# Kernel tuning notes

Hardware: AMD Instinct MI355X
Metric: run time of the kernel (lower is better)

Reference implementation:

```python
import jax, jax.numpy as jnp
import numpy as np

N_NODES = 500_000
N_EDGES = 8_000_000
N_GRAPHS = 25_000
NUM_TASKS = 138
READOUT_DIM = 175
MLP_DIMS = (96, 63)
BN_EPS = 1e-5


def _linear_params(key, fan_in, fan_out):
    k1, k2 = jax.random.split(key)
    bound = 1.0 / np.sqrt(fan_in)
    W = jax.random.uniform(k1, (fan_in, fan_out), jnp.float32, -bound, bound)
    b = jax.random.uniform(k2, (fan_out,), jnp.float32, -bound, bound)
    return W, b


def setup_inputs() -> dict:
    key = jax.random.key(0)
    ks = jax.random.split(key, 16)
    inp = {}
    inp["x"] = jax.random.normal(ks[0], (N_NODES, 48), jnp.float32)
    inp["mol_features"] = jax.random.normal(ks[1], (N_GRAPHS, 10), jnp.float32)
    inp["edge_index"] = jax.random.randint(ks[2], (2, N_EDGES), 0, N_NODES, jnp.int32)
    inp["batch"] = jnp.sort(jax.random.randint(ks[3], (N_NODES,), 0, N_GRAPHS, jnp.int32))
    # GCN layer linears (message transform)
    inp["w_g1"], inp["b_g1"] = _linear_params(ks[4], 48, 20)
    inp["w_g2"], inp["b_g2"] = _linear_params(ks[5], 20, 27)
    inp["w_g3"], inp["b_g3"] = _linear_params(ks[6], 27, 36)
    inp["w_g4"], inp["b_g4"] = _linear_params(ks[7], 36, 36)
    # Readout linears
    inp["w_r1"], inp["b_r1"] = _linear_params(ks[8], 20, READOUT_DIM)
    inp["w_r2"], inp["b_r2"] = _linear_params(ks[9], 27, READOUT_DIM)
    inp["w_r3"], inp["b_r3"] = _linear_params(ks[10], 36, READOUT_DIM)
    inp["w_r4"], inp["b_r4"] = _linear_params(ks[11], 36, READOUT_DIM)
    # MLP
    inp["w_fc1"], inp["b_fc1"] = _linear_params(ks[12], READOUT_DIM + 10, MLP_DIMS[0])
    inp["bn1_g"] = jnp.ones((MLP_DIMS[0],), jnp.float32)
    inp["bn1_b"] = jnp.zeros((MLP_DIMS[0],), jnp.float32)
    inp["w_fc2"], inp["b_fc2"] = _linear_params(ks[13], MLP_DIMS[0], MLP_DIMS[1])
    inp["bn2_g"] = jnp.ones((MLP_DIMS[1],), jnp.float32)
    inp["bn2_b"] = jnp.zeros((MLP_DIMS[1],), jnp.float32)
    inp["w_out"], inp["b_out"] = _linear_params(ks[14], MLP_DIMS[1], NUM_TASKS)
    return inp


def _gcn(x, src, dst, W, b):
    # message: Linear on gathered source features; aggregate: scatter-max; update: SELU
    m = x[src] @ W + b                                  # [E, out]
    agg = jax.ops.segment_max(m, dst, num_segments=N_NODES)
    agg = jnp.where(jnp.isfinite(agg), agg, 0.0)        # PyG fills empty segments with 0
    return jax.nn.selu(agg)


def _readout(x, batch, W, b):
    return jax.ops.segment_sum(x, batch, num_segments=N_GRAPHS) @ W + b


def _bn(h, g, b):
    mu = h.mean(axis=0)
    var = h.var(axis=0)
    return g * (h - mu) / jnp.sqrt(var + BN_EPS) + b


def reference(x, mol_features, w_g1, b_g1, w_g2, b_g2, w_g3, b_g3, w_g4, b_g4,
              w_r1, b_r1, w_r2, b_r2, w_r3, b_r3, w_r4, b_r4,
              w_fc1, b_fc1, bn1_g, bn1_b, w_fc2, b_fc2, bn2_g, bn2_b,
              w_out, b_out, edge_index, batch):
    src, dst = edge_index[0], edge_index[1]
    x1 = _gcn(x, src, dst, w_g1, b_g1)
    x2 = _gcn(x1, src, dst, w_g2, b_g2)
    x3 = _gcn(x2, src, dst, w_g3, b_g3)
    x4 = _gcn(x3, src, dst, w_g4, b_g4)
    r = (_readout(x1, batch, w_r1, b_r1) + _readout(x2, batch, w_r2, b_r2)
         + _readout(x3, batch, w_r3, b_r3) + _readout(x4, batch, w_r4, b_r4))
    h = jnp.concatenate([r, mol_features], axis=1)      # [G, 185]
    h = jax.nn.relu(_bn(h @ w_fc1 + b_fc1, bn1_g, bn1_b))
    h = jax.nn.relu(_bn(h @ w_fc2 + b_fc2, bn2_g, bn2_b))
    return jax.nn.sigmoid(h @ w_out + b_out)            # [G, num_tasks]
```

## Files before the change

### kernel.cpp

```cpp
#include <hip/hip_runtime.h>
#include <hip/hip_fp16.h>
#include <math.h>

#define N_NODES  500000
#define N_EDGES  8000000
#define N_GRAPHS 25000
#define SD  119
#define RD  175
#define H1  96
#define H2  63
#define NT  138
#define GPB 16

#define B2SHIFT 11
#define B2NODES 2048
#define NBUCK2  245
#define BIN_CHUNK 4096
#define NB_BIN 1954
#define NBF 7813
#define CSR_CAP 1536

static __device__ __forceinline__ float selu_f(float m){
    const float scale=1.0507009873554805f, alpha=1.6732632423543772f;
    return m > 0.0f ? scale*m : scale*alpha*(__expf(m)-1.0f);
}

static __device__ __forceinline__ unsigned pkmax(unsigned a, unsigned b){
    unsigned r;
    asm volatile("v_pk_max_f16 %0, %1, %2" : "=v"(r) : "v"(a), "v"(b));
    return r;
}

static __device__ __forceinline__ float2 h2_to_f2(unsigned u){
    union{ unsigned u; __half2 h; } c; c.u = u;
    return __half22float2(c.h);
}

__global__ void k_init(int* chist, float* S){
    int i = blockIdx.x*256 + threadIdx.x;
    if(i < NBUCK2) chist[i] = 0;
    if(i < N_GRAPHS*SD) S[i] = 0.f;
}

__device__ __forceinline__ int block_excl_scan_256(int v){
    __shared__ int sh[256];
    int t = threadIdx.x;
    sh[t] = v; __syncthreads();
    int acc = v;
    for(int off=1; off<256; off<<=1){
        int add = (t>=off) ? sh[t-off] : 0;
        __syncthreads();
        acc += add;
        sh[t] = acc;
        __syncthreads();
    }
    return acc - v;
}

__global__ __launch_bounds__(256) void k_chist(const int* __restrict__ dst, int* __restrict__ chist){
    __shared__ int lh[256];
    int t = threadIdx.x;
    lh[t]=0; __syncthreads();
    int base = blockIdx.x*BIN_CHUNK;
    #pragma unroll
    for(int k=0;k<16;k++){
        int e = base + k*256 + t;
        if(e < N_EDGES) atomicAdd(&lh[dst[e]>>B2SHIFT], 1);
    }
    __syncthreads();
    if(t < NBUCK2 && lh[t]) atomicAdd(&chist[t], lh[t]);
}

__global__ void k_cscan(const int* __restrict__ chist, int* __restrict__ cptr, int* __restrict__ bcur){
    int t = threadIdx.x;
    int v = (t<NBUCK2) ? chist[t] : 0;
    int exc = block_excl_scan_256(v);
    if(t <= NBUCK2) cptr[t] = exc;
    if(t <  NBUCK2) bcur[t] = exc;
}

__global__ __launch_bounds__(256) void k_bin(const int* __restrict__ src, const int* __restrict__ dst,
                                             int* __restrict__ bcur, int* __restrict__ packed){
    __shared__ int   stage[BIN_CHUNK];
    __shared__ unsigned char bkt[BIN_CHUNK];
    __shared__ int lhist[256], lstart[256], lcur[256], gbase[256];
    int t = threadIdx.x;
    int base = blockIdx.x*BIN_CHUNK;
    int myb[16], mys[16];
    #pragma unroll
    for(int k=0;k<16;k++){
        int e = base + k*256 + t;
        if(e < N_EDGES){
            int d = dst[e];
            myb[k] = d >> B2SHIFT;
            mys[k] = ((d & (B2NODES-1)) << 19) | src[e];
        } else myb[k] = -1;
    }
    lhist[t]=0; __syncthreads();
    #pragma unroll
    for(int k=0;k<16;k++) if(myb[k]>=0) atomicAdd(&lhist[myb[k]],1);
    __syncthreads();
    int v = lhist[t];
    int exc = block_excl_scan_256(v);
    lstart[t]=exc; lcur[t]=exc;
    if(t < NBUCK2 && v>0) gbase[t] = atomicAdd(&bcur[t], v);
    __syncthreads();
    #pragma unroll
    for(int k=0;k<16;k++){
        if(myb[k]>=0){
            int p = atomicAdd(&lcur[myb[k]],1);
            stage[p]=mys[k]; bkt[p]=(unsigned char)myb[k];
        }
    }
    __syncthreads();
    int total = N_EDGES - base; if(total > BIN_CHUNK) total = BIN_CHUNK;
    for(int i=t; i<total; i+=256){
        int b = bkt[i];
        packed[gbase[b] + (i - lstart[b])] = stage[i];
    }
}

__global__ __launch_bounds__(1024) void k_scatfine(const int* __restrict__ cptr,
                          const int* __restrict__ packed, int* __restrict__ row_ptr,
                          int* __restrict__ csr){
    __shared__ int cnt[B2NODES];
    __shared__ int sb[1024];
    int t = threadIdx.x;
    int b = blockIdx.x;
    int nb = b << B2SHIFT;
    cnt[t]=0; cnt[t+1024]=0;
    __syncthreads();
    int ebeg = cptr[b], eend = cptr[b+1];
    for(int e=ebeg+t; e<eend; e+=1024){
        int dl = packed[e] >> 19;
        atomicAdd(&cnt[dl],1);
    }
    __syncthreads();
    int c0 = cnt[2*t], c1 = cnt[2*t+1];
    int s = c0+c1;
    sb[t]=s; __syncthreads();
    for(int off=1; off<1024; off<<=1){
        int add = (t>=off) ? sb[t-off] : 0;
        __syncthreads();
        sb[t] += add;
        __syncthreads();
    }
    int excl = sb[t] - s;
    int e0 = excl, e1 = excl + c0;
    __syncthreads();
    cnt[2*t]=e0; cnt[2*t+1]=e1;
    int n0 = nb + 2*t, n1 = nb + 2*t + 1;
    if(n0 < N_NODES) row_ptr[n0] = ebeg + e0;
    if(n1 < N_NODES) row_ptr[n1] = ebeg + e1;
    if(b == NBUCK2-1 && t == 0) row_ptr[N_NODES] = N_EDGES;
    __syncthreads();
    for(int e=ebeg+t; e<eend; e+=1024){
        int v = packed[e];
        int dl = v >> 19;
        int pos = ebeg + atomicAdd(&cnt[dl],1);
        csr[pos] = v & 0x7FFFF;
    }
}

template<int DIN,int DOUT,int PIN,int PH>
__global__ __launch_bounds__(256) void k_transform_h(const float* __restrict__ x, const float* __restrict__ W,
                                                     const float* __restrict__ bias, __half* __restrict__ y){
    __shared__ float swp[PIN*PH];
    __shared__ float sbp[PH];
    int t = threadIdx.x;
    for(int i=t;i<PIN*PH;i+=256){
        int row=i/PH, o=i-row*PH;
        swp[i] = (row<DIN && o<DOUT) ? W[row*DOUT+o] : 0.f;
    }
    if(t<PH) sbp[t] = (t<DOUT) ? bias[t] : 0.f;
    __syncthreads();
    const int TPN = PH/2;
    int gid = blockIdx.x*256 + t;
    if(gid >= N_NODES*TPN) return;
    int n = gid/TPN, op = gid - n*TPN;
    int o0 = 2*op, o1 = o0+1;
    const float4* xr4 = (const float4*)(x + (size_t)n*PIN);
    float acc0 = sbp[o0], acc1 = sbp[o1];
    #pragma unroll
    for(int i4=0;i4<PIN/4;i4++){
        float4 xv = xr4[i4];
        acc0 = fmaf(xv.x, swp[(4*i4+0)*PH+o0], acc0);
        acc1 = fmaf(xv.x, swp[(4*i4+0)*PH+o1], acc1);
        acc0 = fmaf(xv.y, swp[(4*i4+1)*PH+o0], acc0);
        acc1 = fmaf(xv.y, swp[(4*i4+1)*PH+o1], acc1);
        acc0 = fmaf(xv.z, swp[(4*i4+2)*PH+o0], acc0);
        acc1 = fmaf(xv.z, swp[(4*i4+2)*PH+o1], acc1);
        acc0 = fmaf(xv.w, swp[(4*i4+3)*PH+o0], acc0);
        acc1 = fmaf(xv.w, swp[(4*i4+3)*PH+o1], acc1);
    }
    __half2* y2 = (__half2*)y;
    y2[((size_t)n*PH>>1) + op] = __floats2half2_rn(acc0, acc1);
}

template<int FG, class IDX>
static __device__ __forceinline__ void gather_max(const __half* __restrict__ yin,
        IDX idx, int beg, int end, int fg, unsigned m[4]){
    const char* __restrict__ yb = (const char*)yin;
    const unsigned fgo = (unsigned)fg*16u;
    unsigned m0=m[0], m1=m[1], m2=m[2], m3=m[3];
    int j = beg;
    for(; j+8<=end; j+=8){
        int s0=idx(j+0), s1=idx(j+1), s2=idx(j+2), s3=idx(j+3);
        int s4=idx(j+4), s5=idx(j+5), s6=idx(j+6), s7=idx(j+7);
        uint4 v0 = *(const uint4*)(yb + ((unsigned)s0*(FG*16u)+fgo));
        uint4 v1 = *(const uint4*)(yb + ((unsigned)s1*(FG*16u)+fgo));
        uint4 v2 = *(const uint4*)(yb + ((unsigned)s2*(FG*16u)+fgo));
        uint4 v3 = *(const uint4*)(yb + ((unsigned)s3*(FG*16u)+fgo));
        uint4 v4 = *(const uint4*)(yb + ((unsigned)s4*(FG*16u)+fgo));
        uint4 v5 = *(const uint4*)(yb + ((unsigned)s5*(FG*16u)+fgo));
        uint4 v6 = *(const uint4*)(yb + ((unsigned)s6*(FG*16u)+fgo));
        uint4 v7 = *(const uint4*)(yb + ((unsigned)s7*(FG*16u)+fgo));
        m0=pkmax(m0,v0.x); m1=pkmax(m1,v0.y); m2=pkmax(m2,v0.z); m3=pkmax(m3,v0.w);
        m0=pkmax(m0,v1.x); m1=pkmax(m1,v1.y); m2=pkmax(m2,v1.z); m3=pkmax(m3,v1.w);
        m0=pkmax(m0,v2.x); m1=pkmax(m1,v2.y); m2=pkmax(m2,v2.z); m3=pkmax(m3,v2.w);
        m0=pkmax(m0,v3.x); m1=pkmax(m1,v3.y); m2=pkmax(m2,v3.z); m3=pkmax(m3,v3.w);
        m0=pkmax(m0,v4.x); m1=pkmax(m1,v4.y); m2=pkmax(m2,v4.z); m3=pkmax(m3,v4.w);
        m0=pkmax(m0,v5.x); m1=pkmax(m1,v5.y); m2=pkmax(m2,v5.z); m3=pkmax(m3,v5.w);
        m0=pkmax(m0,v6.x); m1=pkmax(m1,v6.y); m2=pkmax(m2,v6.z); m3=pkmax(m3,v6.w);
        m0=pkmax(m0,v7.x); m1=pkmax(m1,v7.y); m2=pkmax(m2,v7.z); m3=pkmax(m3,v7.w);
    }
    for(; j+4<=end; j+=4){
        int s0=idx(j+0), s1=idx(j+1), s2=idx(j+2), s3=idx(j+3);
        uint4 v0 = *(const uint4*)(yb + ((unsigned)s0*(FG*16u)+fgo));
        uint4 v1 = *(const uint4*)(yb + ((unsigned)s1*(FG*16u)+fgo));
        uint4 v2 = *(const uint4*)(yb + ((unsigned)s2*(FG*16u)+fgo));
        uint4 v3 = *(const uint4*)(yb + ((unsigned)s3*(FG*16u)+fgo));
        m0=pkmax(m0,v0.x); m1=pkmax(m1,v0.y); m2=pkmax(m2,v0.z); m3=pkmax(m3,v0.w);
        m0=pkmax(m0,v1.x); m1=pkmax(m1,v1.y); m2=pkmax(m2,v1.z); m3=pkmax(m3,v1.w);
        m0=pkmax(m0,v2.x); m1=pkmax(m1,v2.y); m2=pkmax(m2,v2.z); m3=pkmax(m3,v2.w);
        m0=pkmax(m0,v3.x); m1=pkmax(m1,v3.y); m2=pkmax(m2,v3.z); m3=pkmax(m3,v3.w);
    }
    for(; j<end; j++){
        int s0 = idx(j);
        uint4 v0 = *(const uint4*)(yb + ((unsigned)s0*(FG*16u)+fgo));
        m0=pkmax(m0,v0.x); m1=pkmax(m1,v0.y); m2=pkmax(m2,v0.z); m3=pkmax(m3,v0.w);
    }
    m[0]=m0; m[1]=m1; m[2]=m2; m[3]=m3;
}

static __device__ __forceinline__ void finish_selu(const unsigned m[4], float o[8]){
    float2 f0=h2_to_f2(m[0]), f1=h2_to_f2(m[1]), f2=h2_to_f2(m[2]), f3=h2_to_f2(m[3]);
    float f[8] = {f0.x,f0.y,f1.x,f1.y,f2.x,f2.y,f3.x,f3.y};
    #pragma unroll
    for(int k=0;k<8;k++){
        float v = f[k];
        if(v < -1e30f) v = 0.0f;
        o[k] = selu_f(v);
    }
}

template<int PH_IN,int D_CUR,int SOFF,int D_NEXT,int PH_NEXT>
__global__ __launch_bounds__(64*(PH_IN/8)) void k_fused(
        const __half* __restrict__ yin, const int* __restrict__ row_ptr,
        const int* __restrict__ csr, const int* __restrict__ batch,
        const float* __restrict__ W, const float* __restrict__ bias,
        float* __restrict__ S, __half* __restrict__ yout){
    const int FG = PH_IN/8;
    const int NTH = 64*FG;
    __shared__ float feat[64][PH_IN+1];
    __shared__ float sw[D_CUR*PH_NEXT];
    __shared__ float sb[PH_NEXT];
    __shared__ int sbatch[64];
    __shared__ int scsr[CSR_CAP];
    int t = threadIdx.x;
    int nl = t / FG, fg = t - nl*FG;
    int base = blockIdx.x*64;
    int n = base + nl;
    for(int i=t;i<D_CUR*PH_NEXT;i+=NTH){
        int k=i/PH_NEXT, o2=i-k*PH_NEXT;
        sw[i] = (o2<D_NEXT) ? W[k*D_NEXT+o2] : 0.f;
    }
    if(t<PH_NEXT) sb[t] = (t<D_NEXT) ? bias[t] : 0.f;
    if(t<64) sbatch[t] = (base+t<N_NODES) ? batch[base+t] : -1;
    int nend = base + 64; if(nend > N_NODES) nend = N_NODES;
    int ebeg = row_ptr[base];
    int eblk = row_ptr[nend];
    int nst = eblk - ebeg; if(nst > CSR_CAP) nst = CSR_CAP;
    for(int i=t;i<nst;i+=NTH) scsr[i] = csr[ebeg+i];
    __syncthreads();
    int slim = ebeg + nst;
    float o[8];
    if(n < N_NODES){
        int beg = row_ptr[n], end = row_ptr[n+1];
        unsigned m[4] = {0xFC00FC00u,0xFC00FC00u,0xFC00FC00u,0xFC00FC00u};
        if(end <= slim) gather_max<FG>(yin, [&](int j){ return scsr[j-ebeg]; }, beg, end, fg, m);
        else            gather_max<FG>(yin, [&](int j){ return csr[j]; },       beg, end, fg, m);
        finish_selu(m, o);
    } else {
        for(int k=0;k<8;k++) o[k]=0.f;
    }
    #pragma unroll
    for(int k=0;k<8;k++) feat[nl][8*fg+k] = o[k];
    __syncthreads();
    if(t < D_CUR){
        float acc=0.f; int gprev = sbatch[0];
        for(int mm=0;mm<64;mm++){
            int g = sbatch[mm];
            if(g<0) break;
            if(g!=gprev){ atomicAdd(&S[(size_t)gprev*SD+SOFF+t], acc); acc=0.f; gprev=g; }
            acc += feat[mm][t];
        }
        if(gprev>=0) atomicAdd(&S[(size_t)gprev*SD+SOFF+t], acc);
    }
    if(n < N_NODES){
        for(int o2=fg; o2<PH_NEXT/2; o2+=FG){
            int c0=2*o2, c1=c0+1;
            float a0=sb[c0], a1=sb[c1];
            #pragma unroll
            for(int k=0;k<D_CUR;k++){
                float fv = feat[nl][k];
                a0 = fmaf(fv, sw[k*PH_NEXT+c0], a0);
                a1 = fmaf(fv, sw[k*PH_NEXT+c1], a1);
            }
            ((__half2*)yout)[(size_t)n*(PH_NEXT/2)+o2] = __floats2half2_rn(a0,a1);
        }
    }
}

template<int PH_IN,int D_CUR,int SOFF>
__global__ __launch_bounds__(64*(PH_IN/8)) void k_fused_last(
        const __half* __restrict__ yin, const int* __restrict__ row_ptr,
        const int* __restrict__ csr, const int* __restrict__ batch,
        float* __restrict__ S){
    const int FG = PH_IN/8;
    const int NTH = 64*FG;
    __shared__ float feat[64][PH_IN+1];
    __shared__ int sbatch[64];
    __shared__ int scsr[CSR_CAP];
    int t = threadIdx.x;
    int nl = t / FG, fg = t - nl*FG;
    int base = blockIdx.x*64;
    int n = base + nl;
    if(t<64) sbatch[t] = (base+t<N_NODES) ? batch[base+t] : -1;
    int nend = base + 64; if(nend > N_NODES) nend = N_NODES;
    int ebeg = row_ptr[base];
    int eblk = row_ptr[nend];
    int nst = eblk - ebeg; if(nst > CSR_CAP) nst = CSR_CAP;
    for(int i=t;i<nst;i+=NTH) scsr[i] = csr[ebeg+i];
    __syncthreads();
    int slim = ebeg + nst;
    float o[8];
    if(n < N_NODES){
        int beg = row_ptr[n], end = row_ptr[n+1];
        unsigned m[4] = {0xFC00FC00u,0xFC00FC00u,0xFC00FC00u,0xFC00FC00u};
        if(end <= slim) gather_max<FG>(yin, [&](int j){ return scsr[j-ebeg]; }, beg, end, fg, m);
        else            gather_max<FG>(yin, [&](int j){ return csr[j]; },       beg, end, fg, m);
        finish_selu(m, o);
    } else {
        for(int k=0;k<8;k++) o[k]=0.f;
    }
    #pragma unroll
    for(int k=0;k<8;k++) feat[nl][8*fg+k] = o[k];
    __syncthreads();
    if(t < D_CUR){
        float acc=0.f; int gprev = sbatch[0];
        for(int mm=0;mm<64;mm++){
            int g = sbatch[mm];
            if(g<0) break;
            if(g!=gprev){ atomicAdd(&S[(size_t)gprev*SD+SOFF+t], acc); acc=0.f; gprev=g; }
            acc += feat[mm][t];
        }
        if(gprev>=0) atomicAdd(&S[(size_t)gprev*SD+SOFF+t], acc);
    }
}

__global__ __launch_bounds__(192) void k_readout(const float* __restrict__ S,
    const float* __restrict__ w1,const float* __restrict__ b1,
    const float* __restrict__ w2,const float* __restrict__ b2,
    const float* __restrict__ w3,const float* __restrict__ b3,
    const float* __restrict__ w4,const float* __restrict__ b4,
    float* __restrict__ r){
    __shared__ float sH[GPB][SD];
    int t = threadIdx.x;
    int g0 = blockIdx.x*GPB;
    for(int i=t;i<GPB*SD;i+=192){
        int gl=i/SD, k=i-gl*SD;
        int g=g0+gl;
        sH[gl][k] = (g<N_GRAPHS) ? S[(size_t)g*SD+k] : 0.f;
    }
    __syncthreads();
    int j = t;
    if(j < RD){
        float acc[GPB];
        float bj = b1[j]+b2[j]+b3[j]+b4[j];
        #pragma unroll
        for(int gl=0;gl<GPB;gl++) acc[gl]=bj;
        for(int k=0;k<20;k++){ float wv=w1[k*RD+j];
            #pragma unroll
            for(int gl=0;gl<GPB;gl++) acc[gl] += sH[gl][k]*wv; }
        for(int k=0;k<27;k++){ float wv=w2[k*RD+j];
            #pragma unroll
            for(int gl=0;gl<GPB;gl++) acc[gl] += sH[gl][20+k]*wv; }
        for(int k=0;k<36;k++){ float wv=w3[k*RD+j];
            #pragma unroll
            for(int gl=0;gl<GPB;gl++) acc[gl] += sH[gl][47+k]*wv; }
        for(int k=0;k<36;k++){ float wv=w4[k*RD+j];
            #pragma unroll
            for(int gl=0;gl<GPB;gl++) acc[gl] += sH[gl][83+k]*wv; }
        int ng = min(GPB, N_GRAPHS-g0);
        for(int gl=0;gl<ng;gl++) r[(size_t)(g0+gl)*RD+j] = acc[gl];
    }
}

__global__ __launch_bounds__(128) void k_fc1(const float* __restrict__ r, const float* __restrict__ mol,
    const float* __restrict__ w, const float* __restrict__ b,
    float* __restrict__ z1, float* __restrict__ ps, float* __restrict__ pq){
    __shared__ float sH[GPB][RD+10];
    int t = threadIdx.x;
    int g0 = blockIdx.x*GPB;
    for(int i=t;i<GPB*(RD+10);i+=128){
        int gl=i/(RD+10), k=i-gl*(RD+10);
        int g=g0+gl;
        float v=0.f;
        if(g<N_GRAPHS) v = (k<RD) ? r[(size_t)g*RD+k] : mol[(size_t)g*10 + (k-RD)];
        sH[gl][k]=v;
    }
    __syncthreads();
    int j = t;
    if(j < H1){
        float acc[GPB]; float bj=b[j];
        #pragma unroll
        for(int gl=0;gl<GPB;gl++) acc[gl]=bj;
        for(int k=0;k<RD+10;k++){
            float wv = w[k*H1+j];
            #pragma unroll
            for(int gl=0;gl<GPB;gl++) acc[gl] += sH[gl][k]*wv;
        }
        int ng = min(GPB, N_GRAPHS-g0);
        float psum=0.f, psq=0.f;
        for(int gl=0;gl<ng;gl++){
            z1[(size_t)(g0+gl)*H1+j]=acc[gl];
            psum+=acc[gl]; psq+=acc[gl]*acc[gl];
        }
        ps[blockIdx.x*H1+j]=psum;
        pq[blockIdx.x*H1+j]=psq;
    }
}

__global__ __launch_bounds__(256) void k_bnfin(const float* __restrict__ ps, const float* __restrict__ pq,
    int nb, int H, const float* __restrict__ gamma, const float* __restrict__ beta,
    float* __restrict__ a, float* __restrict__ c){
    int j = blockIdx.x;
    int t = threadIdx.x;
    float s=0.f, q=0.f;
    for(int i=t;i<nb;i+=256){ s+=ps[(size_t)i*H+j]; q+=pq[(size_t)i*H+j]; }
    __shared__ float sh1[256], sh2[256];
    sh1[t]=s; sh2[t]=q; __syncthreads();
    for(int off=128;off>0;off>>=1){
        if(t<off){ sh1[t]+=sh1[t+off]; sh2[t]+=sh2[t+off]; }
        __syncthreads();
    }
    if(t==0){
        float mean = sh1[0]/(float)N_GRAPHS;
        float var  = sh2[0]/(float)N_GRAPHS - mean*mean;
        float inv  = 1.0f/sqrtf(var + 1e-5f);
        float aj = gamma[j]*inv;
        a[j]=aj; c[j]=beta[j]-aj*mean;
    }
}

__global__ __launch_bounds__(64) void k_fc2(const float* __restrict__ z1, const float* __restrict__ a1,
    const float* __restrict__ c1, const float* __restrict__ w, const float* __restrict__ b,
    float* __restrict__ z2, float* __restrict__ ps, float* __restrict__ pq){
    __shared__ float sH[GPB][H1];
    int t = threadIdx.x;
    int g0 = blockIdx.x*GPB;
    for(int i=t;i<GPB*H1;i+=64){
        int gl=i/H1, k=i-gl*H1;
        int g=g0+gl;
        float v=0.f;
        if(g<N_GRAPHS){ float z=z1[(size_t)g*H1+k]; v=fmaxf(a1[k]*z+c1[k],0.f); }
        sH[gl][k]=v;
    }
    __syncthreads();
    int j = t;
    if(j < H2){
        float acc[GPB]; float bj=b[j];
        #pragma unroll
        for(int gl=0;gl<GPB;gl++) acc[gl]=bj;
        for(int k=0;k<H1;k++){
            float wv=w[k*H2+j];
            #pragma unroll
            for(int gl=0;gl<GPB;gl++) acc[gl]+=sH[gl][k]*wv;
        }
        int ng=min(GPB,N_GRAPHS-g0);
        float psum=0.f,psq=0.f;
        for(int gl=0;gl<ng;gl++){
            z2[(size_t)(g0+gl)*H2+j]=acc[gl];
            psum+=acc[gl]; psq+=acc[gl]*acc[gl];
        }
        ps[blockIdx.x*H2+j]=psum; pq[blockIdx.x*H2+j]=psq;
    }
}

__global__ __launch_bounds__(192) void k_out(const float* __restrict__ z2, const float* __restrict__ a2,
    const float* __restrict__ c2, const float* __restrict__ w, const float* __restrict__ b,
    float* __restrict__ out){
    __shared__ float sH[GPB][H2];
    int t = threadIdx.x;
    int g0 = blockIdx.x*GPB;
    for(int i=t;i<GPB*H2;i+=192){
        int gl=i/H2, k=i-gl*H2;
        int g=g0+gl;
        float v=0.f;
        if(g<N_GRAPHS){ float z=z2[(size_t)g*H2+k]; v=fmaxf(a2[k]*z+c2[k],0.f); }
        sH[gl][k]=v;
    }
    __syncthreads();
    int j = t;
    if(j < NT){
        float acc[GPB]; float bj=b[j];
        #pragma unroll
        for(int gl=0;gl<GPB;gl++) acc[gl]=bj;
        for(int k=0;k<H2;k++){
            float wv=w[k*NT+j];
            #pragma unroll
            for(int gl=0;gl<GPB;gl++) acc[gl]+=sH[gl][k]*wv;
        }
        int ng=min(GPB,N_GRAPHS-g0);
        for(int gl=0;gl<ng;gl++)
            out[(size_t)(g0+gl)*NT+j] = 1.0f/(1.0f+__expf(-acc[gl]));
    }
}

static inline int ceil_div(int a,int b){ return (a+b-1)/b; }

extern "C" void kernel_launch(void* const* d_in, const int* in_sizes, int n_in,
                              void* d_out, int out_size, void* d_ws, size_t ws_size,
                              hipStream_t stream) {
    const float* x     = (const float*)d_in[0];
    const float* mol   = (const float*)d_in[1];
    const int*   ei    = (const int*)  d_in[2];
    const int*   batch = (const int*)  d_in[3];
    const float* w_g1=(const float*)d_in[4];  const float* b_g1=(const float*)d_in[5];
    const float* w_g2=(const float*)d_in[6];  const float* b_g2=(const float*)d_in[7];
    const float* w_g3=(const float*)d_in[8];  const float* b_g3=(const float*)d_in[9];
    const float* w_g4=(const float*)d_in[10]; const float* b_g4=(const float*)d_in[11];
    const float* w_r1=(const float*)d_in[12]; const float* b_r1=(const float*)d_in[13];
    const float* w_r2=(const float*)d_in[14]; const float* b_r2=(const float*)d_in[15];
    const float* w_r3=(const float*)d_in[16]; const float* b_r3=(const float*)d_in[17];
    const float* w_r4=(const float*)d_in[18]; const float* b_r4=(const float*)d_in[19];
    const float* w_fc1=(const float*)d_in[20]; const float* b_fc1=(const float*)d_in[21];
    const float* bn1_g=(const float*)d_in[22]; const float* bn1_b=(const float*)d_in[23];
    const float* w_fc2=(const float*)d_in[24]; const float* b_fc2=(const float*)d_in[25];
    const float* bn2_g=(const float*)d_in[26]; const float* bn2_b=(const float*)d_in[27];
    const float* w_out=(const float*)d_in[28]; const float* b_out=(const float*)d_in[29];
    float* out = (float*)d_out;

    char* p = (char*)d_ws;
    auto take=[&](size_t bytes)->char*{ char* q=p; p += (bytes+255)&~(size_t)255; return q; };
    __half* yA = (__half*)take((size_t)N_NODES*40*2);
    __half* yB = (__half*)take((size_t)N_NODES*40*2);
    int* chist   = (int*)take((size_t)NBUCK2*4);
    int* cptr    = (int*)take((size_t)(NBUCK2+1)*4);
    int* bcur    = (int*)take((size_t)NBUCK2*4);
    int* row_ptr = (int*)take((size_t)(N_NODES+1)*4);
    int* packed  = (int*)take((size_t)N_EDGES*4);
    int* csr     = (int*)take((size_t)N_EDGES*4);
    float* S  = (float*)take((size_t)N_GRAPHS*SD*4);
    float* r  = (float*)take((size_t)N_GRAPHS*RD*4);
    float* z1 = (float*)take((size_t)N_GRAPHS*H1*4);
    float* z2 = (float*)take((size_t)N_GRAPHS*H2*4);
    const int NB_G = ceil_div(N_GRAPHS, GPB);
    float* p1s=(float*)take((size_t)NB_G*H1*4);
    float* p1q=(float*)take((size_t)NB_G*H1*4);
    float* p2s=(float*)take((size_t)NB_G*H2*4);
    float* p2q=(float*)take((size_t)NB_G*H2*4);
    float* a1=(float*)take(H1*4); float* c1=(float*)take(H1*4);
    float* a2=(float*)take(H2*4); float* c2=(float*)take(H2*4);

    const int* src = ei;
    const int* dst = ei + N_EDGES;

    k_init<<<ceil_div(N_GRAPHS*SD,256),256,0,stream>>>(chist,S);
    k_chist<<<NB_BIN,256,0,stream>>>(dst,chist);
    k_cscan<<<1,256,0,stream>>>(chist,cptr,bcur);
    k_bin<<<NB_BIN,256,0,stream>>>(src,dst,bcur,packed);
    k_scatfine<<<NBUCK2,1024,0,stream>>>(cptr,packed,row_ptr,csr);

    k_transform_h<48,20,48,24><<<ceil_div(N_NODES*12,256),256,0,stream>>>(x,w_g1,b_g1,yA);
    k_fused<24,20,0, 27,32><<<NBF,192,0,stream>>>(yA,row_ptr,csr,batch,w_g2,b_g2,S,yB);
    k_fused<32,27,20,36,40><<<NBF,256,0,stream>>>(yB,row_ptr,csr,batch,w_g3,b_g3,S,yA);
    k_fused<40,36,47,36,40><<<NBF,320,0,stream>>>(yA,row_ptr,csr,batch,w_g4,b_g4,S,yB);
    k_fused_last<40,36,83><<<NBF,320,0,stream>>>(yB,row_ptr,csr,batch,S);

    k_readout<<<NB_G,192,0,stream>>>(S,w_r1,b_r1,w_r2,b_r2,w_r3,b_r3,w_r4,b_r4,r);
    k_fc1<<<NB_G,128,0,stream>>>(r,mol,w_fc1,b_fc1,z1,p1s,p1q);
    k_bnfin<<<H1,256,0,stream>>>(p1s,p1q,NB_G,H1,bn1_g,bn1_b,a1,c1);
    k_fc2<<<NB_G,64,0,stream>>>(z1,a1,c1,w_fc2,b_fc2,z2,p2s,p2q);
    k_bnfin<<<H2,256,0,stream>>>(p2s,p2q,NB_G,H2,bn2_g,bn2_b,a2,c2);
    k_out<<<NB_G,192,0,stream>>>(z2,a2,c2,w_out,b_out,out);
}
```

Baseline: 1.426 ms.

## Sort each node's CSR neighbors by source chunk and gather chunk-by-chunk

The fine scatter pass now keys each edge by destination node plus the top bits of its source index, one of 8 chunks of 65536 nodes. Each node's neighbor list therefore comes out grouped by source region. The fused gather kernels walk these runs chunk by chunk, so concurrent lanes tend to read nearby parts of the feature table, which is meant to improve cache locality. In exchange the histogram shared memory grows 8x, a serial run-length scan is added per node, and the 8-wide unrolled gather loop is removed, which cuts memory-level parallelism for short runs.

```diff
diff --git a/kernel.cpp b/kernel.cpp
--- a/kernel.cpp
+++ b/kernel.cpp
@@ -19,6 +19,7 @@
 #define NB_BIN 1954
 #define NBF 7813
 #define CSR_CAP 1536
+#define NCH 8
 
 static __device__ __forceinline__ float selu_f(float m){
     const float scale=1.0507009873554805f, alpha=1.6732632423543772f;
@@ -123,41 +124,48 @@
 __global__ __launch_bounds__(1024) void k_scatfine(const int* __restrict__ cptr,
                           const int* __restrict__ packed, int* __restrict__ row_ptr,
                           int* __restrict__ csr){
-    __shared__ int cnt[B2NODES];
+    __shared__ int cnt[B2NODES*NCH];
     __shared__ int sb[1024];
     int t = threadIdx.x;
     int b = blockIdx.x;
     int nb = b << B2SHIFT;
-    cnt[t]=0; cnt[t+1024]=0;
+    for(int i=t;i<B2NODES*NCH;i+=1024) cnt[i]=0;
     __syncthreads();
     int ebeg = cptr[b], eend = cptr[b+1];
     for(int e=ebeg+t; e<eend; e+=1024){
-        int dl = packed[e] >> 19;
-        atomicAdd(&cnt[dl],1);
-    }
-    __syncthreads();
-    int c0 = cnt[2*t], c1 = cnt[2*t+1];
-    int s = c0+c1;
-    sb[t]=s; __syncthreads();
+        int v = packed[e];
+        int key = ((v>>19)<<3) | ((v & 0x7FFFF) >> 16);
+        atomicAdd(&cnt[key],1);
+    }
+    __syncthreads();
+    int c[16]; int S=0;
+    #pragma unroll
+    for(int k=0;k<16;k++){ c[k]=cnt[16*t+k]; S+=c[k]; }
+    sb[t]=S; __syncthreads();
     for(int off=1; off<1024; off<<=1){
         int add = (t>=off) ? sb[t-off] : 0;
         __syncthreads();
         sb[t] += add;
         __syncthreads();
     }
-    int excl = sb[t] - s;
-    int e0 = excl, e1 = excl + c0;
-    __syncthreads();
-    cnt[2*t]=e0; cnt[2*t+1]=e1;
+    int excl = sb[t] - S;
+    int run = excl, start0 = 0, start8 = 0;
+    #pragma unroll
+    for(int k=0;k<16;k++){
+        if(k==0) start0 = run;
+        if(k==8) start8 = run;
+        cnt[16*t+k] = run;
+        run += c[k];
+    }
     int n0 = nb + 2*t, n1 = nb + 2*t + 1;
-    if(n0 < N_NODES) row_ptr[n0] = ebeg + e0;
-    if(n1 < N_NODES) row_ptr[n1] = ebeg + e1;
+    if(n0 < N_NODES) row_ptr[n0] = ebeg + start0;
+    if(n1 < N_NODES) row_ptr[n1] = ebeg + start8;
     if(b == NBUCK2-1 && t == 0) row_ptr[N_NODES] = N_EDGES;
     __syncthreads();
     for(int e=ebeg+t; e<eend; e+=1024){
         int v = packed[e];
-        int dl = v >> 19;
-        int pos = ebeg + atomicAdd(&cnt[dl],1);
+        int key = ((v>>19)<<3) | ((v & 0x7FFFF) >> 16);
+        int pos = ebeg + atomicAdd(&cnt[key],1);
         csr[pos] = v & 0x7FFFF;
     }
 }
@@ -204,26 +212,6 @@
     const unsigned fgo = (unsigned)fg*16u;
     unsigned m0=m[0], m1=m[1], m2=m[2], m3=m[3];
     int j = beg;
-    for(; j+8<=end; j+=8){
-        int s0=idx(j+0), s1=idx(j+1), s2=idx(j+2), s3=idx(j+3);
-        int s4=idx(j+4), s5=idx(j+5), s6=idx(j+6), s7=idx(j+7);
-        uint4 v0 = *(const uint4*)(yb + ((unsigned)s0*(FG*16u)+fgo));
-        uint4 v1 = *(const uint4*)(yb + ((unsigned)s1*(FG*16u)+fgo));
-        uint4 v2 = *(const uint4*)(yb + ((unsigned)s2*(FG*16u)+fgo));
-        uint4 v3 = *(const uint4*)(yb + ((unsigned)s3*(FG*16u)+fgo));
-        uint4 v4 = *(const uint4*)(yb + ((unsigned)s4*(FG*16u)+fgo));
-        uint4 v5 = *(const uint4*)(yb + ((unsigned)s5*(FG*16u)+fgo));
-        uint4 v6 = *(const uint4*)(yb + ((unsigned)s6*(FG*16u)+fgo));
-        uint4 v7 = *(const uint4*)(yb + ((unsigned)s7*(FG*16u)+fgo));
-        m0=pkmax(m0,v0.x); m1=pkmax(m1,v0.y); m2=pkmax(m2,v0.z); m3=pkmax(m3,v0.w);
-        m0=pkmax(m0,v1.x); m1=pkmax(m1,v1.y); m2=pkmax(m2,v1.z); m3=pkmax(m3,v1.w);
-        m0=pkmax(m0,v2.x); m1=pkmax(m1,v2.y); m2=pkmax(m2,v2.z); m3=pkmax(m3,v2.w);
-        m0=pkmax(m0,v3.x); m1=pkmax(m1,v3.y); m2=pkmax(m2,v3.z); m3=pkmax(m3,v3.w);
-        m0=pkmax(m0,v4.x); m1=pkmax(m1,v4.y); m2=pkmax(m2,v4.z); m3=pkmax(m3,v4.w);
-        m0=pkmax(m0,v5.x); m1=pkmax(m1,v5.y); m2=pkmax(m2,v5.z); m3=pkmax(m3,v5.w);
-        m0=pkmax(m0,v6.x); m1=pkmax(m1,v6.y); m2=pkmax(m2,v6.z); m3=pkmax(m3,v6.w);
-        m0=pkmax(m0,v7.x); m1=pkmax(m1,v7.y); m2=pkmax(m2,v7.z); m3=pkmax(m3,v7.w);
-    }
     for(; j+4<=end; j+=4){
         int s0=idx(j+0), s1=idx(j+1), s2=idx(j+2), s3=idx(j+3);
         uint4 v0 = *(const uint4*)(yb + ((unsigned)s0*(FG*16u)+fgo));
@@ -241,6 +229,20 @@
         m0=pkmax(m0,v0.x); m1=pkmax(m1,v0.y); m2=pkmax(m2,v0.z); m3=pkmax(m3,v0.w);
     }
     m[0]=m0; m[1]=m1; m[2]=m2; m[3]=m3;
+}
+
+template<int FG, class IDX>
+static __device__ __forceinline__ void gather_max_chunked(const __half* __restrict__ yin,
+        IDX idx, int beg, int end, int fg, unsigned m[4]){
+    int j = beg;
+    #pragma unroll 1
+    for(int c=0;c<NCH;c++){
+        int run = 0;
+        while(j+run < end && (idx(j+run)>>16) == c) run++;
+        if(run) gather_max<FG>(yin, idx, j, j+run, fg, m);
+        j += run;
+        if(j >= end) break;
+    }
 }
 
 static __device__ __forceinline__ void finish_selu(const unsigned m[4], float o[8]){
@@ -288,8 +290,8 @@
     if(n < N_NODES){
         int beg = row_ptr[n], end = row_ptr[n+1];
         unsigned m[4] = {0xFC00FC00u,0xFC00FC00u,0xFC00FC00u,0xFC00FC00u};
-        if(end <= slim) gather_max<FG>(yin, [&](int j){ return scsr[j-ebeg]; }, beg, end, fg, m);
-        else            gather_max<FG>(yin, [&](int j){ return csr[j]; },       beg, end, fg, m);
+        if(end <= slim) gather_max_chunked<FG>(yin, [&](int j){ return scsr[j-ebeg]; }, beg, end, fg, m);
+        else            gather_max_chunked<FG>(yin, [&](int j){ return csr[j]; },       beg, end, fg, m);
         finish_selu(m, o);
     } else {
         for(int k=0;k<8;k++) o[k]=0.f;
@@ -348,8 +350,8 @@
     if(n < N_NODES){
         int beg = row_ptr[n], end = row_ptr[n+1];
         unsigned m[4] = {0xFC00FC00u,0xFC00FC00u,0xFC00FC00u,0xFC00FC00u};
-        if(end <= slim) gather_max<FG>(yin, [&](int j){ return scsr[j-ebeg]; }, beg, end, fg, m);
-        else            gather_max<FG>(yin, [&](int j){ return csr[j]; },       beg, end, fg, m);
+        if(end <= slim) gather_max_chunked<FG>(yin, [&](int j){ return scsr[j-ebeg]; }, beg, end, fg, m);
+        else            gather_max_chunked<FG>(yin, [&](int j){ return csr[j]; },       beg, end, fg, m);
         finish_selu(m, o);
     } else {
         for(int k=0;k<8;k++) o[k]=0.f;
```

After: 1.561 ms. 1.09x slower.

## Shrink fp16 node-feature row padding and gather with overlapping 16-byte chunks

Applied to the files above, without the earlier changes.

Feature rows in the intermediate fp16 buffers are now stored with smaller padding (40/56/72 bytes instead of 48/64/80), so each gathered row carries fewer wasted bytes. The last thread group of each node reads an overlapping 16-byte chunk at the row end, and the vector type is relaxed to 8-byte alignment so unaligned row strides still work. This cuts gather traffic in the memory-bound scatter-max layers. In exchange, the 16-byte loads can straddle cache lines and are split into smaller transactions, and the overlapping chunk duplicates a few loads and shared-memory writes.

```diff
diff --git a/kernel.cpp b/kernel.cpp
--- a/kernel.cpp
+++ b/kernel.cpp
@@ -35,6 +35,8 @@
     union{ unsigned u; __half2 h; } c; c.u = u;
     return __half22float2(c.h);
 }
+
+struct __align__(8) U4 { unsigned x, y, z, w; };
 
 __global__ void k_init(int* chist, float* S){
     int i = blockIdx.x*256 + threadIdx.x;
@@ -194,27 +196,26 @@
         acc1 = fmaf(xv.w, swp[(4*i4+3)*PH+o1], acc1);
     }
     __half2* y2 = (__half2*)y;
-    y2[((size_t)n*PH>>1) + op] = __floats2half2_rn(acc0, acc1);
-}
-
-template<int FG, class IDX>
+    y2[(size_t)n*TPN + op] = __floats2half2_rn(acc0, acc1);
+}
+
+template<int ROWB, class IDX>
 static __device__ __forceinline__ void gather_max(const __half* __restrict__ yin,
-        IDX idx, int beg, int end, int fg, unsigned m[4]){
+        IDX idx, int beg, int end, unsigned offb, unsigned m[4]){
     const char* __restrict__ yb = (const char*)yin;
-    const unsigned fgo = (unsigned)fg*16u;
     unsigned m0=m[0], m1=m[1], m2=m[2], m3=m[3];
     int j = beg;
     for(; j+8<=end; j+=8){
         int s0=idx(j+0), s1=idx(j+1), s2=idx(j+2), s3=idx(j+3);
         int s4=idx(j+4), s5=idx(j+5), s6=idx(j+6), s7=idx(j+7);
-        uint4 v0 = *(const uint4*)(yb + ((unsigned)s0*(FG*16u)+fgo));
-        uint4 v1 = *(const uint4*)(yb + ((unsigned)s1*(FG*16u)+fgo));
-        uint4 v2 = *(const uint4*)(yb + ((unsigned)s2*(FG*16u)+fgo));
-        uint4 v3 = *(const uint4*)(yb + ((unsigned)s3*(FG*16u)+fgo));
-        uint4 v4 = *(const uint4*)(yb + ((unsigned)s4*(FG*16u)+fgo));
-        uint4 v5 = *(const uint4*)(yb + ((unsigned)s5*(FG*16u)+fgo));
-        uint4 v6 = *(const uint4*)(yb + ((unsigned)s6*(FG*16u)+fgo));
-        uint4 v7 = *(const uint4*)(yb + ((unsigned)s7*(FG*16u)+fgo));
+        U4 v0 = *(const U4*)(yb + ((unsigned)s0*(unsigned)ROWB + offb));
+        U4 v1 = *(const U4*)(yb + ((unsigned)s1*(unsigned)ROWB + offb));
+        U4 v2 = *(const U4*)(yb + ((unsigned)s2*(unsigned)ROWB + offb));
+        U4 v3 = *(const U4*)(yb + ((unsigned)s3*(unsigned)ROWB + offb));
+        U4 v4 = *(const U4*)(yb + ((unsigned)s4*(unsigned)ROWB + offb));
+        U4 v5 = *(const U4*)(yb + ((unsigned)s5*(unsigned)ROWB + offb));
+        U4 v6 = *(const U4*)(yb + ((unsigned)s6*(unsigned)ROWB + offb));
+        U4 v7 = *(const U4*)(yb + ((unsigned)s7*(unsigned)ROWB + offb));
         m0=pkmax(m0,v0.x); m1=pkmax(m1,v0.y); m2=pkmax(m2,v0.z); m3=pkmax(m3,v0.w);
         m0=pkmax(m0,v1.x); m1=pkmax(m1,v1.y); m2=pkmax(m2,v1.z); m3=pkmax(m3,v1.w);
         m0=pkmax(m0,v2.x); m1=pkmax(m1,v2.y); m2=pkmax(m2,v2.z); m3=pkmax(m3,v2.w);
@@ -226,10 +227,10 @@
     }
     for(; j+4<=end; j+=4){
         int s0=idx(j+0), s1=idx(j+1), s2=idx(j+2), s3=idx(j+3);
-        uint4 v0 = *(const uint4*)(yb + ((unsigned)s0*(FG*16u)+fgo));
-        uint4 v1 = *(const uint4*)(yb + ((unsigned)s1*(FG*16u)+fgo));
-        uint4 v2 = *(const uint4*)(yb + ((unsigned)s2*(FG*16u)+fgo));
-        uint4 v3 = *(const uint4*)(yb + ((unsigned)s3*(FG*16u)+fgo));
+        U4 v0 = *(const U4*)(yb + ((unsigned)s0*(unsigned)ROWB + offb));
+        U4 v1 = *(const U4*)(yb + ((unsigned)s1*(unsigned)ROWB + offb));
+        U4 v2 = *(const U4*)(yb + ((unsigned)s2*(unsigned)ROWB + offb));
+        U4 v3 = *(const U4*)(yb + ((unsigned)s3*(unsigned)ROWB + offb));
         m0=pkmax(m0,v0.x); m1=pkmax(m1,v0.y); m2=pkmax(m2,v0.z); m3=pkmax(m3,v0.w);
         m0=pkmax(m0,v1.x); m1=pkmax(m1,v1.y); m2=pkmax(m2,v1.z); m3=pkmax(m3,v1.w);
         m0=pkmax(m0,v2.x); m1=pkmax(m1,v2.y); m2=pkmax(m2,v2.z); m3=pkmax(m3,v2.w);
@@ -237,7 +238,7 @@
     }
     for(; j<end; j++){
         int s0 = idx(j);
-        uint4 v0 = *(const uint4*)(yb + ((unsigned)s0*(FG*16u)+fgo));
+        U4 v0 = *(const U4*)(yb + ((unsigned)s0*(unsigned)ROWB + offb));
         m0=pkmax(m0,v0.x); m1=pkmax(m1,v0.y); m2=pkmax(m2,v0.z); m3=pkmax(m3,v0.w);
     }
     m[0]=m0; m[1]=m1; m[2]=m2; m[3]=m3;
@@ -254,28 +255,30 @@
     }
 }
 
-template<int PH_IN,int D_CUR,int SOFF,int D_NEXT,int PH_NEXT>
-__global__ __launch_bounds__(64*(PH_IN/8)) void k_fused(
+template<int ROWB_IN,int D_CUR,int SOFF,int D_NEXT,int ROWB_NEXT>
+__global__ __launch_bounds__(64*(ROWB_IN/16+1)) void k_fused(
         const __half* __restrict__ yin, const int* __restrict__ row_ptr,
         const int* __restrict__ csr, const int* __restrict__ batch,
         const float* __restrict__ W, const float* __restrict__ bias,
         float* __restrict__ S, __half* __restrict__ yout){
-    const int FG = PH_IN/8;
+    const int FG  = ROWB_IN/16 + 1;
     const int NTH = 64*FG;
-    __shared__ float feat[64][PH_IN+1];
-    __shared__ float sw[D_CUR*PH_NEXT];
-    __shared__ float sb[PH_NEXT];
+    const int NF  = ROWB_IN/2;
+    const int OH  = ROWB_NEXT/2;
+    __shared__ float feat[64][NF+1];
+    __shared__ float sw[D_CUR*OH];
+    __shared__ float sb[OH];
     __shared__ int sbatch[64];
     __shared__ int scsr[CSR_CAP];
     int t = threadIdx.x;
     int nl = t / FG, fg = t - nl*FG;
     int base = blockIdx.x*64;
     int n = base + nl;
-    for(int i=t;i<D_CUR*PH_NEXT;i+=NTH){
-        int k=i/PH_NEXT, o2=i-k*PH_NEXT;
+    for(int i=t;i<D_CUR*OH;i+=NTH){
+        int k=i/OH, o2=i-k*OH;
         sw[i] = (o2<D_NEXT) ? W[k*D_NEXT+o2] : 0.f;
     }
-    if(t<PH_NEXT) sb[t] = (t<D_NEXT) ? bias[t] : 0.f;
+    if(t<OH) sb[t] = (t<D_NEXT) ? bias[t] : 0.f;
     if(t<64) sbatch[t] = (base+t<N_NODES) ? batch[base+t] : -1;
     int nend = base + 64; if(nend > N_NODES) nend = N_NODES;
     int ebeg = row_ptr[base];
@@ -284,18 +287,20 @@
     for(int i=t;i<nst;i+=NTH) scsr[i] = csr[ebeg+i];
     __syncthreads();
     int slim = ebeg + nst;
+    unsigned offb = (unsigned)(fg*16 < ROWB_IN-16 ? fg*16 : ROWB_IN-16);
     float o[8];
     if(n < N_NODES){
         int beg = row_ptr[n], end = row_ptr[n+1];
         unsigned m[4] = {0xFC00FC00u,0xFC00FC00u,0xFC00FC00u,0xFC00FC00u};
-        if(end <= slim) gather_max<FG>(yin, [&](int j){ return scsr[j-ebeg]; }, beg, end, fg, m);
-        else            gather_max<FG>(yin, [&](int j){ return csr[j]; },       beg, end, fg, m);
+        if(end <= slim) gather_max<ROWB_IN>(yin, [&](int j){ return scsr[j-ebeg]; }, beg, end, offb, m);
+        else            gather_max<ROWB_IN>(yin, [&](int j){ return csr[j]; },       beg, end, offb, m);
         finish_selu(m, o);
     } else {
         for(int k=0;k<8;k++) o[k]=0.f;
     }
-    #pragma unroll
-    for(int k=0;k<8;k++) feat[nl][8*fg+k] = o[k];
+    int offh = (int)(offb>>1);
+    #pragma unroll
+    for(int k=0;k<8;k++) feat[nl][offh+k] = o[k];
     __syncthreads();
     if(t < D_CUR){
         float acc=0.f; int gprev = sbatch[0];
@@ -308,28 +313,29 @@
         if(gprev>=0) atomicAdd(&S[(size_t)gprev*SD+SOFF+t], acc);
     }
     if(n < N_NODES){
-        for(int o2=fg; o2<PH_NEXT/2; o2+=FG){
+        for(int o2=fg; o2<OH/2; o2+=FG){
             int c0=2*o2, c1=c0+1;
             float a0=sb[c0], a1=sb[c1];
             #pragma unroll
             for(int k=0;k<D_CUR;k++){
                 float fv = feat[nl][k];
-                a0 = fmaf(fv, sw[k*PH_NEXT+c0], a0);
-                a1 = fmaf(fv, sw[k*PH_NEXT+c1], a1);
+                a0 = fmaf(fv, sw[k*OH+c0], a0);
+                a1 = fmaf(fv, sw[k*OH+c1], a1);
             }
-            ((__half2*)yout)[(size_t)n*(PH_NEXT/2)+o2] = __floats2half2_rn(a0,a1);
-        }
-    }
-}
-
-template<int PH_IN,int D_CUR,int SOFF>
-__global__ __launch_bounds__(64*(PH_IN/8)) void k_fused_last(
+            ((__half2*)yout)[(size_t)n*(OH/2)+o2] = __floats2half2_rn(a0,a1);
+        }
+    }
+}
+
+template<int ROWB_IN,int D_CUR,int SOFF>
+__global__ __launch_bounds__(64*(ROWB_IN/16+1)) void k_fused_last(
         const __half* __restrict__ yin, const int* __restrict__ row_ptr,
         const int* __restrict__ csr, const int* __restrict__ batch,
         float* __restrict__ S){
-    const int FG = PH_IN/8;
+    const int FG  = ROWB_IN/16 + 1;
     const int NTH = 64*FG;
-    __shared__ float feat[64][PH_IN+1];
+    const int NF  = ROWB_IN/2;
+    __shared__ float feat[64][NF+1];
     __shared__ int sbatch[64];
     __shared__ int scsr[CSR_CAP];
     int t = threadIdx.x;
@@ -344,18 +350,20 @@
     for(int i=t;i<nst;i+=NTH) scsr[i] = csr[ebeg+i];
     __syncthreads();
     int slim = ebeg + nst;
+    unsigned offb = (unsigned)(fg*16 < ROWB_IN-16 ? fg*16 : ROWB_IN-16);
     float o[8];
     if(n < N_NODES){
         int beg = row_ptr[n], end = row_ptr[n+1];
         unsigned m[4] = {0xFC00FC00u,0xFC00FC00u,0xFC00FC00u,0xFC00FC00u};
-        if(end <= slim) gather_max<FG>(yin, [&](int j){ return scsr[j-ebeg]; }, beg, end, fg, m);
-        else            gather_max<FG>(yin, [&](int j){ return csr[j]; },       beg, end, fg, m);
+        if(end <= slim) gather_max<ROWB_IN>(yin, [&](int j){ return scsr[j-ebeg]; }, beg, end, offb, m);
+        else            gather_max<ROWB_IN>(yin, [&](int j){ return csr[j]; },       beg, end, offb, m);
         finish_selu(m, o);
     } else {
         for(int k=0;k<8;k++) o[k]=0.f;
     }
-    #pragma unroll
-    for(int k=0;k<8;k++) feat[nl][8*fg+k] = o[k];
+    int offh = (int)(offb>>1);
+    #pragma unroll
+    for(int k=0;k<8;k++) feat[nl][offh+k] = o[k];
     __syncthreads();
     if(t < D_CUR){
         float acc=0.f; int gprev = sbatch[0];
@@ -554,8 +562,8 @@
 
     char* p = (char*)d_ws;
     auto take=[&](size_t bytes)->char*{ char* q=p; p += (bytes+255)&~(size_t)255; return q; };
-    __half* yA = (__half*)take((size_t)N_NODES*40*2);
-    __half* yB = (__half*)take((size_t)N_NODES*40*2);
+    __half* yA = (__half*)take((size_t)N_NODES*72 + 256);
+    __half* yB = (__half*)take((size_t)N_NODES*72 + 256);
     int* chist   = (int*)take((size_t)NBUCK2*4);
     int* cptr    = (int*)take((size_t)(NBUCK2+1)*4);
     int* bcur    = (int*)take((size_t)NBUCK2*4);
@@ -583,11 +591,11 @@
     k_bin<<<NB_BIN,256,0,stream>>>(src,dst,bcur,packed);
     k_scatfine<<<NBUCK2,1024,0,stream>>>(cptr,packed,row_ptr,csr);
 
-    k_transform_h<48,20,48,24><<<ceil_div(N_NODES*12,256),256,0,stream>>>(x,w_g1,b_g1,yA);
-    k_fused<24,20,0, 27,32><<<NBF,192,0,stream>>>(yA,row_ptr,csr,batch,w_g2,b_g2,S,yB);
-    k_fused<32,27,20,36,40><<<NBF,256,0,stream>>>(yB,row_ptr,csr,batch,w_g3,b_g3,S,yA);
-    k_fused<40,36,47,36,40><<<NBF,320,0,stream>>>(yA,row_ptr,csr,batch,w_g4,b_g4,S,yB);
-    k_fused_last<40,36,83><<<NBF,320,0,stream>>>(yB,row_ptr,csr,batch,S);
+    k_transform_h<48,20,48,20><<<ceil_div(N_NODES*10,256),256,0,stream>>>(x,w_g1,b_g1,yA);
+    k_fused<40,20,0, 27,56><<<NBF,192,0,stream>>>(yA,row_ptr,csr,batch,w_g2,b_g2,S,yB);
+    k_fused<56,27,20,36,72><<<NBF,256,0,stream>>>(yB,row_ptr,csr,batch,w_g3,b_g3,S,yA);
+    k_fused<72,36,47,36,72><<<NBF,320,0,stream>>>(yA,row_ptr,csr,batch,w_g4,b_g4,S,yB);
+    k_fused_last<72,36,83><<<NBF,320,0,stream>>>(yB,row_ptr,csr,batch,S);
 
     k_readout<<<NB_G,192,0,stream>>>(S,w_r1,b_r1,w_r2,b_r2,w_r3,b_r3,w_r4,b_r4,r);
     k_fc1<<<NB_G,128,0,stream>>>(r,mol,w_fc1,b_fc1,z1,p1s,p1q);
```

After: 1.427 ms. About the same (+0.1%).
